# Optimization experiments

Measured on AMD Instinct MI355X. Metric: run time of the kernel, lower is better.

## Reference

```python
import jax, jax.numpy as jnp
import numpy as np

B, N, C, H = 32, 512, 1024, 16
HD = C // H  # head_dim = 64
SCALE = HD ** -0.5


def setup_inputs() -> dict:
    key = jax.random.key(0)
    k1, k2, k3, k4 = jax.random.split(key, 4)
    # xavier_uniform bounds
    qkv_bound = (6.0 / (C + 3 * C)) ** 0.5
    proj_bound = 1.414 * (6.0 / (C + C)) ** 0.5
    return {
        "x": jax.random.normal(k1, (B, N, C), dtype=jnp.float32),
        "mask": jax.random.uniform(k2, (B, N), dtype=jnp.float32),
        "W_qkv": jax.random.uniform(k3, (3 * C, C), dtype=jnp.float32, minval=-qkv_bound, maxval=qkv_bound),
        "W_proj": jax.random.uniform(k4, (C, C), dtype=jnp.float32, minval=-proj_bound, maxval=proj_bound),
        "b_proj": jnp.zeros((C,), dtype=jnp.float32),
    }


def reference(x, mask, W_qkv, W_proj, b_proj):
    # qkv projection (no bias): [B,N,3C] -> [3,B,H,N,HD]
    qkv = jnp.einsum("bnc,dc->bnd", x, W_qkv)
    qkv = qkv.reshape(B, N, 3, H, HD).transpose(2, 0, 3, 1, 4)
    q, k, v = qkv[0] * SCALE, qkv[1], qkv[2]
    # attention scores [B,H,N,N] with additive row/col mask bias
    attn = jnp.einsum("bhqd,bhkd->bhqk", q, k)
    attn = attn + mask[:, None, None, :] + mask[:, None, :, None]
    attn = jax.nn.softmax(attn, axis=-1)
    out = jnp.einsum("bhqk,bhkd->bhqd", attn, v)
    out = out.transpose(0, 2, 1, 3).reshape(B, N, C)
    return jnp.einsum("bnc,dc->bnd", out, W_proj) + b_proj
```

## Files before the change

### kernel.cpp

```cpp
#include <hip/hip_runtime.h>
#include <stdint.h>

typedef unsigned short u16;
typedef __bf16 bf16x8 __attribute__((ext_vector_type(8)));
typedef float  f32x4  __attribute__((ext_vector_type(4)));
typedef float  f32x16 __attribute__((ext_vector_type(16)));
typedef unsigned int u32x4 __attribute__((ext_vector_type(4)));

#define MFMA16(a,b,c) __builtin_amdgcn_mfma_f32_16x16x32_bf16((a),(b),(c),0,0,0)
#define MFMA32(a,b,c) __builtin_amdgcn_mfma_f32_32x32x16_bf16((a),(b),(c),0,0,0)

#if __has_builtin(__builtin_amdgcn_exp2f)
#define EXP2F(x) __builtin_amdgcn_exp2f(x)
#else
#define EXP2F(x) exp2f(x)
#endif

__device__ __forceinline__ u16 f2b(float f) {
  unsigned int u = __builtin_bit_cast(unsigned int, f);
  u += 0x7fffu + ((u >> 16) & 1u);
  return (u16)(u >> 16);
}

__device__ __forceinline__ void gll16(const u16* g, u16* l) {
  __builtin_amdgcn_global_load_lds((const __attribute__((address_space(1))) unsigned int*)g,
                                   (__attribute__((address_space(3))) unsigned int*)l,
                                   16, 0, 0);
}

__device__ __forceinline__ unsigned cvtpk(float lo, float hi) {
  unsigned r;
  asm("v_cvt_pk_bf16_f32 %0, %1, %2" : "=v"(r) : "v"(lo), "v"(hi));
  return r;
}
__device__ __forceinline__ void pl32swap(unsigned &x, unsigned &y) {
  asm volatile("v_permlane32_swap_b32 %0, %1" : "+v"(x), "+v"(y));
}

#define BARR() __builtin_amdgcn_s_barrier()
#define LGKM0() do { asm volatile("s_waitcnt lgkmcnt(0)" ::: "memory"); __builtin_amdgcn_sched_barrier(0); } while (0)
#define VMC(N) asm volatile("s_waitcnt vmcnt(" #N ")" ::: "memory")
#define PRIO1() __builtin_amdgcn_s_setprio(1)
#define PRIO0() __builtin_amdgcn_s_setprio(0)

__global__ __launch_bounds__(256)
void cvt_all(const float* __restrict__ X, const float* __restrict__ Wq,
             const float* __restrict__ Wp, u16* __restrict__ Xb,
             u16* __restrict__ Wqb, u16* __restrict__ Wpb)
{
  size_t i = (size_t)blockIdx.x * 256 + threadIdx.x;
  const float* src; u16* dst; size_t off;
  if (i < 4194304)       { src = X;  dst = Xb;  off = i; }
  else if (i < 4980736)  { src = Wq; dst = Wqb; off = i - 4194304; }
  else                   { src = Wp; dst = Wpb; off = i - 4980736; }
  float4 v = ((const float4*)src)[off];
  uint2 p;
  p.x = f2b(v.x) | ((unsigned)f2b(v.y) << 16);
  p.y = f2b(v.z) | ((unsigned)f2b(v.w) << 16);
  ((uint2*)dst)[off] = p;
}

#define DS_A(CUR, AF, RBASE) do { \
  _Pragma("unroll") for (int mt = 0; mt < 4; mt++) \
  _Pragma("unroll") for (int ks = 0; ks < 2; ks++) \
    AF[mt][ks] = *(const bf16x8*)((const char*)Asmem[CUR] + (RBASE) + aoff[mt][ks]); \
} while (0)

#define DS_B2(CUR, N0) do { \
  _Pragma("unroll") for (int nt = 0; nt < 2; nt++) \
  _Pragma("unroll") for (int ks = 0; ks < 2; ks++) \
    bfr[(N0) + nt][ks] = *(const bf16x8*)((const char*)Bsmem[CUR] + boff[(N0) + nt][ks]); \
} while (0)

#define MQ(MB, NB, AF) do { \
  _Pragma("unroll") for (int mt = 0; mt < 4; mt++) \
  _Pragma("unroll") for (int nt = 0; nt < 2; nt++) \
  _Pragma("unroll") for (int ks = 0; ks < 2; ks++) \
    acc[(MB) + mt][(NB) + nt] = MFMA16(AF[mt][ks], bfr[(NB) + nt][ks], acc[(MB) + mt][(NB) + nt]); \
} while (0)

#define HALF_ITER(CUR, TA, TB, ENDW) do { \
   \
  DS_A(CUR, afl, 0); DS_B2(CUR, 0); \
  STAGE_A(TA, 0); \
  BARR(); LGKM0(); \
  PRIO1(); MQ(0, 0, afl); PRIO0(); \
  BARR(); \
   \
  DS_B2(CUR, 2); \
  STAGE_A(TA, 1); \
  BARR(); LGKM0(); \
  PRIO1(); MQ(0, 2, afl); PRIO0(); \
  BARR(); \
   \
  DS_A(CUR, afh, 8192); \
  STAGE_B(TB, 0); \
  BARR(); LGKM0(); \
  PRIO1(); MQ(4, 0, afh); PRIO0(); \
  BARR(); \
   \
  STAGE_B(TB, 1); \
  PRIO1(); MQ(4, 2, afh); PRIO0(); \
  ENDW; \
  BARR(); \
} while (0)

template <int EPI>
__global__ __launch_bounds__(512, 2)
void gemm8p(const u16* __restrict__ Ag, const u16* __restrict__ Wg,
            u16* __restrict__ qb, u16* __restrict__ kb, u16* __restrict__ vT,
            const float* __restrict__ bias, float* __restrict__ outf, int nbx)
{
  __shared__ u16 Asmem[2][16384];
  __shared__ u16 Bsmem[2][16384];

  const int nwg = gridDim.x;
  const int cpx = nwg >> 3;
  const int bid = blockIdx.x;
  const int wg  = (bid & 7) * cpx + (bid >> 3);
  const int bx = wg % nbx, by = wg / nbx;
  const int row0 = by * 256, col0 = bx * 256;

  const int t = threadIdx.x;
  const int lane = t & 63, w = t >> 6;
  const int quad = lane >> 4, l16 = lane & 15;
  const int wm = w >> 2, wn = w & 3;
  const int sx = l16 & 7;

  const int srow = lane >> 3;
  const int scol = ((lane & 7) ^ srow) * 8;
  const u16* pA0 = Ag + (size_t)(row0 + w * 16 + srow) * 1024 + scol;
  const u16* pB0 = Wg + (size_t)(col0 + w * 16 + srow) * 1024 + scol;

  int aoff[4][2], boff[4][2];
#pragma unroll
  for (int mt = 0; mt < 4; mt++)
#pragma unroll
    for (int ks = 0; ks < 2; ks++) {
      int r = wm * 128 + mt * 16 + l16;
      aoff[mt][ks] = r * 128 + (((ks * 4 + quad) ^ sx) * 16);
    }
#pragma unroll
  for (int nt = 0; nt < 4; nt++)
#pragma unroll
    for (int ks = 0; ks < 2; ks++) {
      int r = wn * 64 + nt * 16 + l16;
      boff[nt][ks] = r * 128 + (((ks * 4 + quad) ^ sx) * 16);
    }

  f32x4 acc[8][4];
#pragma unroll
  for (int i = 0; i < 8; i++)
#pragma unroll
    for (int j = 0; j < 4; j++) acc[i][j] = f32x4{0.f, 0.f, 0.f, 0.f};

  auto STAGE_A = [&](int tile, int half) {
    if (tile >= 16) return;
    const u16* g = pA0 + (size_t)half * 131072 + tile * 64;
    u16* l = &Asmem[tile & 1][(half * 128 + w * 16) * 64];
    gll16(g, l);
    gll16(g + 8192, l + 512);
  };
  auto STAGE_B = [&](int tile, int half) {
    if (tile >= 16) return;
    const u16* g = pB0 + (size_t)half * 131072 + tile * 64;
    u16* l = &Bsmem[tile & 1][(half * 128 + w * 16) * 64];
    gll16(g, l);
    gll16(g + 8192, l + 512);
  };

  bf16x8 afl[4][2], afh[4][2], bfr[4][2];

  STAGE_B(0, 0); STAGE_B(0, 1); STAGE_A(0, 0); STAGE_A(0, 1);
  STAGE_B(1, 0); STAGE_B(1, 1);
  VMC(4); BARR();

  for (int i = 0; i < 7; ++i) {
    int t1 = 2 * i + 1;
    HALF_ITER(0, t1, t1 + 1, VMC(4));
    HALF_ITER(1, t1 + 1, t1 + 2, VMC(4));
  }
  HALF_ITER(0, 15, 16, VMC(0));
  HALF_ITER(1, 16, 17, ((void)0));

  const int tok_base = row0 + wm * 128;
  if constexpr (EPI == 0) {
#pragma unroll
    for (int nt = 0; nt < 4; nt++) {
      int d = col0 + wn * 64 + nt * 16;
      int part = d >> 10;
      int hh = (d >> 6) & 15;
      int hd = (d & 63) + l16;
      if (part == 2) {
#pragma unroll
        for (int mt = 0; mt < 8; mt++) {
          int nb = tok_base + mt * 16 + quad * 4;
          int bb = nb >> 9, nn = nb & 511;
          uint2 pk;
          pk.x = f2b(acc[mt][nt][0]) | ((unsigned)f2b(acc[mt][nt][1]) << 16);
          pk.y = f2b(acc[mt][nt][2]) | ((unsigned)f2b(acc[mt][nt][3]) << 16);
          *(uint2*)(vT + (((size_t)(bb * 16 + hh)) * 64 + hd) * 512 + nn) = pk;
        }
      } else {
        u16* dst = (part == 0) ? qb : kb;
        float sc = (part == 0) ? 0.125f : 1.0f;
#pragma unroll
        for (int mt = 0; mt < 8; mt++)
#pragma unroll
          for (int r = 0; r < 4; r++) {
            int tok = tok_base + mt * 16 + quad * 4 + r;
            int bb = tok >> 9, nn = tok & 511;
            dst[(((size_t)(bb * 16 + hh)) * 512 + nn) * 64 + hd] = f2b(acc[mt][nt][r] * sc);
          }
      }
    }
  } else {
#pragma unroll
    for (int nt = 0; nt < 4; nt++) {
      int d = col0 + wn * 64 + nt * 16 + l16;
      float bv = bias[d];
#pragma unroll
      for (int mt = 0; mt < 8; mt++)
#pragma unroll
        for (int r = 0; r < 4; r++) {
          int tok = tok_base + mt * 16 + quad * 4 + r;
          outf[(size_t)tok * 1024 + d] = acc[mt][nt][r] + bv;
        }
    }
  }
}

__global__ __launch_bounds__(256)
void attn_kernel(const u16* __restrict__ qb, const u16* __restrict__ kb,
                 const u16* __restrict__ vT, const float* __restrict__ mask,
                 u16* __restrict__ ao)
{
  __shared__ u16 Kbuf[2][64 * 64];
  __shared__ u16 Vbuf[2][64 * 64];
  __shared__ float mk2[512];
  __shared__ float Lbuf[128];

  const int bid = blockIdx.x;
  const int wid = (bid & 7) * 256 + (bid >> 3);
  const int qt = wid & 3, bh = wid >> 2;
  const int b = bh >> 4, hh = bh & 15;

  const int t = threadIdx.x;
  const int lane = t & 63, w = t >> 6;
  const int l31 = lane & 31, hi = lane >> 5;
  const int sw = l31 & 7;

  const u16* Qp = qb + (size_t)bh * 512 * 64;
  const u16* Kp = kb + (size_t)bh * 512 * 64;
  const u16* Vp = vT + (size_t)bh * 64 * 512;

  for (int i = t; i < 512; i += 256) mk2[i] = mask[b * 512 + i] * 1.44269504f;

  const int qbase = qt * 128 + w * 32;
  bf16x8 qf[4];
#pragma unroll
  for (int dc = 0; dc < 4; dc++)
    qf[dc] = *(const bf16x8*)(Qp + (size_t)(qbase + l31) * 64 + dc * 16 + hi * 8);

  const int sr = lane >> 3, sc = lane & 7;
  const int cg = sc ^ sr;
  const u16* gk[2]; const u16* gv[2];
#pragma unroll
  for (int j = 0; j < 2; j++) {
    int r = w * 16 + j * 8 + sr;
    gk[j] = Kp + (size_t)r * 64 + cg * 8;
    gv[j] = Vp + (size_t)r * 512 + cg * 8;
  }

  f32x16 oacc[2];
#pragma unroll
  for (int i = 0; i < 16; i++) { oacc[0][i] = 0.f; oacc[1][i] = 0.f; }
  float lsum = 0.f;

  auto STAGE = [&](int tt, int buf) {
#pragma unroll
    for (int j = 0; j < 2; j++) {
      gll16(gk[j] + (size_t)tt * 4096, &Kbuf[buf][(w * 16 + j * 8) * 64]);
      gll16(gv[j] + (size_t)tt * 64,   &Vbuf[buf][(w * 16 + j * 8) * 64]);
    }
  };

  STAGE(0, 0);
  __syncthreads();

  for (int tt = 0; tt < 8; tt++) {
    const int cur = tt & 1;
    if (tt < 7) STAGE(tt + 1, cur ^ 1);
    const u16* Kb = Kbuf[cur];
    const u16* Vb = Vbuf[cur];
#pragma unroll
    for (int c = 0; c < 2; c++) {
      f32x16 s;
#pragma unroll
      for (int i = 0; i < 16; i++) s[i] = 0.f;
#pragma unroll
      for (int dc = 0; dc < 4; dc++) {
        int row = c * 32 + l31;
        bf16x8 kf = *(const bf16x8*)((const char*)Kb + row * 128 + (((2 * dc + hi) ^ sw) * 16));
        s = MFMA32(kf, qf[dc], s);
      }
      const int kb0 = tt * 64 + c * 32;
      f32x4 mkv[4];
#pragma unroll
      for (int g = 0; g < 4; g++) mkv[g] = *(const f32x4*)(mk2 + kb0 + g * 8 + hi * 4);
      float p[16];
#pragma unroll
      for (int r = 0; r < 16; r++)
        p[r] = EXP2F(fmaf(s[r], 1.44269504f, mkv[r >> 2][r & 3]));
      float ls = 0.f;
#pragma unroll
      for (int r = 0; r < 16; r++) ls += p[r];
      lsum += ls;

      unsigned d0a = cvtpk(p[0],  p[1]),  d1a = cvtpk(p[2],  p[3]);
      unsigned d2a = cvtpk(p[4],  p[5]),  d3a = cvtpk(p[6],  p[7]);
      unsigned d0b = cvtpk(p[8],  p[9]),  d1b = cvtpk(p[10], p[11]);
      unsigned d2b = cvtpk(p[12], p[13]), d3b = cvtpk(p[14], p[15]);
      pl32swap(d0a, d2a);
      pl32swap(d1a, d3a);
      pl32swap(d0b, d2b);
      pl32swap(d1b, d3b);
      u32x4 w0; w0.x = d0a; w0.y = d1a; w0.z = d2a; w0.w = d3a;
      u32x4 w1; w1.x = d0b; w1.y = d1b; w1.z = d2b; w1.w = d3b;
      bf16x8 af[2];
      af[0] = __builtin_bit_cast(bf16x8, w0);
      af[1] = __builtin_bit_cast(bf16x8, w1);

#pragma unroll
      for (int kc = 0; kc < 2; kc++)
#pragma unroll
        for (int dc = 0; dc < 2; dc++) {
          int row = dc * 32 + l31;
          bf16x8 vf = *(const bf16x8*)((const char*)Vb + row * 128 + (((4 * c + 2 * kc + hi) ^ sw) * 16));
          oacc[dc] = MFMA32(af[kc], vf, oacc[dc]);
        }
    }
    __syncthreads();
  }

  lsum += __shfl_xor(lsum, 32);
  if (lane < 32) Lbuf[w * 32 + l31] = 1.0f / lsum;
  __syncthreads();
  f32x4 inv4[4];
#pragma unroll
  for (int g = 0; g < 4; g++) inv4[g] = *(const f32x4*)(Lbuf + w * 32 + g * 8 + hi * 4);

#pragma unroll
  for (int dc = 0; dc < 2; dc++)
#pragma unroll
    for (int r = 0; r < 16; r++) {
      int qrow = (r & 3) + 8 * (r >> 2) + 4 * hi;
      int n = qbase + qrow;
      int col = hh * 64 + dc * 32 + l31;
      ao[((size_t)(b * 512 + n)) * 1024 + col] = f2b(oacc[dc][r] * inv4[r >> 2][r & 3]);
    }
}

extern "C" void kernel_launch(void* const* d_in, const int* in_sizes, int n_in,
                              void* d_out, int out_size, void* d_ws, size_t ws_size,
                              hipStream_t stream) {
  const float* x     = (const float*)d_in[0];
  const float* mask  = (const float*)d_in[1];
  const float* Wqkv  = (const float*)d_in[2];
  const float* Wproj = (const float*)d_in[3];
  const float* bproj = (const float*)d_in[4];
  float* out = (float*)d_out;

  u16* qb  = (u16*)d_ws;
  u16* kb  = qb + 16777216;
  u16* vT  = kb + 16777216;
  u16* XbAo = vT + 16777216;
  u16* Wqb = XbAo + 16777216;
  u16* Wpb = Wqb + 3145728;

  cvt_all<<<20480, 256, 0, stream>>>(x, Wqkv, Wproj, XbAo, Wqb, Wpb);
  gemm8p<0><<<768, 512, 0, stream>>>(XbAo, Wqb, qb, kb, vT, nullptr, nullptr, 12);
  attn_kernel<<<2048, 256, 0, stream>>>(qb, kb, vT, mask, XbAo);
  gemm8p<1><<<256, 512, 0, stream>>>(XbAo, Wpb, nullptr, nullptr, nullptr, bproj, out, 4);
}
```

Before: 340.3 us.

## Issue all LDS fragment reads up front and overlap MFMAs via partial lgkmcnt waits

The GEMM half-iteration is reordered so that every LDS fragment read for the stage is issued at once, followed by the global->LDS staging loads. Partial lgkmcnt waits then let each MFMA group start as soon as its own operands have arrived, rather than waiting on a full drain. The number of workgroup barriers per half-iteration drops from seven to two. The main loop is also kept rolled and sched_barriers are added around waits to pin the order. In exchange, more fragment registers stay live at once, and correctness now depends on LDS reads returning in order and on the single barrier that guards the B-buffer overwrite.

Measured after the change: 331.2 us. 2.7% less time.

```diff
diff --git a/kernel.cpp b/kernel.cpp
--- a/kernel.cpp
+++ b/kernel.cpp
@@ -38,8 +38,9 @@
 }
 
 #define BARR() __builtin_amdgcn_s_barrier()
-#define LGKM0() do { asm volatile("s_waitcnt lgkmcnt(0)" ::: "memory"); __builtin_amdgcn_sched_barrier(0); } while (0)
-#define VMC(N) asm volatile("s_waitcnt vmcnt(" #N ")" ::: "memory")
+#define SCHED0() __builtin_amdgcn_sched_barrier(0)
+#define LGKM(N) do { asm volatile("s_waitcnt lgkmcnt(" #N ")" ::: "memory"); __builtin_amdgcn_sched_barrier(0); } while (0)
+#define VMC(N) do { asm volatile("s_waitcnt vmcnt(" #N ")" ::: "memory"); __builtin_amdgcn_sched_barrier(0); } while (0)
 #define PRIO1() __builtin_amdgcn_s_setprio(1)
 #define PRIO0() __builtin_amdgcn_s_setprio(0)
 
@@ -81,26 +82,15 @@
 
 #define HALF_ITER(CUR, TA, TB, ENDW) do { \
    \
-  DS_A(CUR, afl, 0); DS_B2(CUR, 0); \
-  STAGE_A(TA, 0); \
-  BARR(); LGKM0(); \
-  PRIO1(); MQ(0, 0, afl); PRIO0(); \
-  BARR(); \
-   \
-  DS_B2(CUR, 2); \
-  STAGE_A(TA, 1); \
-  BARR(); LGKM0(); \
-  PRIO1(); MQ(0, 2, afl); PRIO0(); \
-  BARR(); \
-   \
-  DS_A(CUR, afh, 8192); \
-  STAGE_B(TB, 0); \
-  BARR(); LGKM0(); \
-  PRIO1(); MQ(4, 0, afh); PRIO0(); \
-  BARR(); \
-   \
-  STAGE_B(TB, 1); \
-  PRIO1(); MQ(4, 2, afh); PRIO0(); \
+  DS_A(CUR, afl, 0); DS_B2(CUR, 0); SCHED0(); \
+  DS_B2(CUR, 2); SCHED0(); \
+  DS_A(CUR, afh, 8192); SCHED0(); \
+  STAGE_A(TA, 0); STAGE_A(TA, 1); \
+  LGKM(12); PRIO1(); MQ(0, 0, afl); PRIO0(); \
+  LGKM(8);  PRIO1(); MQ(0, 2, afl); PRIO0(); \
+  BARR();   \
+  STAGE_B(TB, 0); STAGE_B(TB, 1); \
+  LGKM(0);  PRIO1(); MQ(4, 0, afh); MQ(4, 2, afh); PRIO0(); \
   ENDW; \
   BARR(); \
 } while (0)
@@ -172,9 +162,11 @@
   bf16x8 afl[4][2], afh[4][2], bfr[4][2];
 
   STAGE_B(0, 0); STAGE_B(0, 1); STAGE_A(0, 0); STAGE_A(0, 1);
+  SCHED0();
   STAGE_B(1, 0); STAGE_B(1, 1);
   VMC(4); BARR();
 
+#pragma unroll 1
   for (int i = 0; i < 7; ++i) {
     int t1 = 2 * i + 1;
     HALF_ITER(0, t1, t1 + 1, VMC(4));
```
